# Kernel tuning notes

Hardware: AMD Instinct MI355X
Metric: run time of the kernel (lower is better)

## Reference

```python
import jax, jax.numpy as jnp
import numpy as np

DIM = 512
HEADS = 8
DIM_HEAD = 64
HIDDEN = HEADS * DIM_HEAD  # 512
SCALE = DIM_HEAD ** -0.5


def setup_inputs() -> dict:
    key = jax.random.key(0)
    k1, k2, k3 = jax.random.split(key, 3)
    x = jax.random.normal(k1, (4, 2048, DIM), dtype=jnp.float32)
    # torch Linear weight convention: [out_features, in_features], y = x @ W.T
    W_qkv = jax.random.normal(k2, (3 * HIDDEN, DIM), dtype=jnp.float32) * (DIM ** -0.5)
    W_out = jax.random.normal(k3, (DIM, HIDDEN), dtype=jnp.float32) * (HIDDEN ** -0.5)
    return {"x": x, "W_qkv": W_qkv, "W_out": W_out}


def reference(x, W_qkv, W_out):
    b, n, c = x.shape
    qkv = jnp.einsum('bnc,oc->bno', x, W_qkv)  # [b, n, 3*hidden]
    q, k, v = jnp.split(qkv, 3, axis=-1)
    # rearrange 'b n (h c) -> b h c n'
    def to_heads(t):
        return jnp.transpose(t.reshape(b, n, HEADS, DIM_HEAD), (0, 2, 3, 1))
    q, k, v = to_heads(q), to_heads(k), to_heads(v)
    q = q * SCALE
    sim = jnp.einsum('bhcn,bhcj->bhnj', q, k)  # [b, h, n, n]
    attn = jax.nn.softmax(sim, axis=-1)
    out = jnp.einsum('bhnj,bhdj->bhnd', attn, v)  # [b, h, n, d]
    out = jnp.transpose(out, (0, 2, 1, 3)).reshape(b, n, HIDDEN)  # 'b h n d -> b n (h d)'
    return jnp.einsum('bnh,oh->bno', out, W_out)
```

## Files before the change

kernel.cpp:

```cpp
#include <hip/hip_runtime.h>


typedef unsigned short u16;
typedef __attribute__((ext_vector_type(8))) short s16x8;
typedef __attribute__((ext_vector_type(4))) float f32x4;
typedef __attribute__((ext_vector_type(16))) float f32x16;

__device__ __forceinline__ u16 f2bf(float f) {
  unsigned int u = __float_as_uint(f);
  u = (u + 0x7fffu + ((u >> 16) & 1u)) >> 16;
  return (u16)u;
}

__device__ __forceinline__ void gload16(const u16* g, u16* lds_base) {
  __builtin_amdgcn_global_load_lds(
      (const __attribute__((address_space(1))) unsigned int*)g,
      (__attribute__((address_space(3))) unsigned int*)lds_base, 16, 0, 0);
}

__device__ __forceinline__ void permlane32_swap(unsigned& a, unsigned& b) {
  asm volatile("v_permlane32_swap_b32 %0, %1" : "+v"(a), "+v"(b));
}

__global__ __launch_bounds__(256) void cvt_all(
    const float* __restrict__ x, const float* __restrict__ w1,
    const float* __restrict__ w2, u16* __restrict__ xb,
    u16* __restrict__ w1b, u16* __restrict__ w2b) {
  constexpr int N1 = 8192 * 512 / 4, N2 = 1536 * 512 / 4, N3 = 512 * 512 / 4;
  int i = blockIdx.x * 256 + threadIdx.x;
  if (i >= N1 + N2 + N3) return;
  const float* src;
  u16* dst;
  int j;
  if (i < N1) { src = x; dst = xb; j = i; }
  else if (i < N1 + N2) { src = w1; dst = w1b; j = i - N1; }
  else { src = w2; dst = w2b; j = i - N1 - N2; }
  float4 f = ((const float4*)src)[j];
  uint2 o;
  o.x = (unsigned)f2bf(f.x) | ((unsigned)f2bf(f.y) << 16);
  o.y = (unsigned)f2bf(f.z) | ((unsigned)f2bf(f.w) << 16);
  ((uint2*)dst)[j] = o;
}

template <int BN, int MODE>
__global__ __launch_bounds__(256) void gemm128(
    const u16* __restrict__ A, const u16* __restrict__ B,
    float* __restrict__ Cf,
    u16* __restrict__ Qp, u16* __restrict__ Kp, u16* __restrict__ Vp) {
  constexpr int K = 512;
  constexpr int JN = BN / 32;
  __shared__ u16 smem[128 * 64 + BN * 64];
  u16* As = smem;
  u16* Bs = smem + 128 * 64;
  const int bm0 = blockIdx.x * 128, bn0 = blockIdx.y * BN;
  const int t = threadIdx.x, wave = t >> 6, lane = t & 63;
  const int quad = lane >> 4, l16 = lane & 15;
  const int wm = (wave & 1) * 64, wn = (wave >> 1) * (BN / 2);
  const int lr = lane >> 3, lc = lane & 7;
  const int swz = lc ^ lr;

  f32x4 acc[4][JN] = {};

  for (int k0 = 0; k0 < K; k0 += 64) {
    __syncthreads();
#pragma unroll
    for (int a = 0; a < 4; a++) {
      int r = wave * 32 + a * 8 + lr;
      gload16(A + (size_t)(bm0 + r) * K + k0 + swz * 8,
              &As[(wave * 32 + a * 8) * 64]);
    }
#pragma unroll
    for (int b = 0; b < BN / 32; b++) {
      int r = wave * (BN / 4) + b * 8 + lr;
      gload16(B + (size_t)(bn0 + r) * K + k0 + swz * 8,
              &Bs[(wave * (BN / 4) + b * 8) * 64]);
    }
    __syncthreads();
#pragma unroll
    for (int ks = 0; ks < 2; ks++) {
      s16x8 af[4], bf[JN];
#pragma unroll
      for (int i = 0; i < 4; i++) {
        int m = wm + i * 16 + l16;
        af[i] = *(const s16x8*)(&As[m * 64 + (((ks * 4 + quad) ^ (m & 7)) * 8)]);
      }
#pragma unroll
      for (int j = 0; j < JN; j++) {
        int n = wn + j * 16 + l16;
        bf[j] = *(const s16x8*)(&Bs[n * 64 + (((ks * 4 + quad) ^ (n & 7)) * 8)]);
      }
#pragma unroll
      for (int i = 0; i < 4; i++)
#pragma unroll
        for (int j = 0; j < JN; j++)
          acc[i][j] = __builtin_amdgcn_mfma_f32_16x16x32_bf16(af[i], bf[j], acc[i][j], 0, 0, 0);
    }
  }

  if constexpr (MODE == 1) {
#pragma unroll
    for (int i = 0; i < 4; i++)
#pragma unroll
      for (int j = 0; j < JN; j++)
#pragma unroll
        for (int r = 0; r < 4; r++) {
          int m = bm0 + wm + i * 16 + quad * 4 + r;
          int n = bn0 + wn + j * 16 + l16;
          Cf[(size_t)m * 512 + n] = acc[i][j][r];
        }
  } else {
    const int part = bn0 >> 9;
    if (part < 2) {
#pragma unroll
      for (int i = 0; i < 4; i++)
#pragma unroll
        for (int j = 0; j < JN; j++)
#pragma unroll
          for (int r = 0; r < 4; r++) {
            int m = bm0 + wm + i * 16 + quad * 4 + r;
            int n = bn0 + wn + j * 16 + l16;
            int oin = n & 511;
            int head = oin >> 6, dh = oin & 63;
            int bb = m >> 11, tok = m & 2047;
            size_t idx = ((size_t)(bb * 8 + head) * 2048 + tok) * 64 + dh;
            if (part == 0)
              Qp[idx] = f2bf(acc[i][j][r] * 0.18033688011112042f);
            else
              Kp[idx] = f2bf(acc[i][j][r]);
          }
    } else {
      __syncthreads();
#pragma unroll
      for (int i = 0; i < 4; i++)
#pragma unroll
        for (int j = 0; j < JN; j++)
#pragma unroll
          for (int r = 0; r < 4; r++) {
            int row = wm + i * 16 + quad * 4 + r;
            int cn = wn + j * 16 + l16;
            smem[row * 128 + (cn ^ (row & 7))] = f2bf(acc[i][j][r]);
          }
      __syncthreads();
      const int bb = bm0 >> 11;
      const int tokbase = bm0 & 2047;
      const int headbase = (bn0 & 511) >> 6;
#pragma unroll
      for (int it = 0; it < 8; it++) {
        int cn = it * 16 + (t >> 4);
        int dh = cn & 63, head = headbase + (cn >> 6);
        int tok0 = (t & 15) * 8;
        s16x8 pk;
#pragma unroll
        for (int k = 0; k < 8; k++) {
          int row = tok0 + k;
          pk[k] = (short)smem[row * 128 + (cn ^ (row & 7))];
        }
        *(s16x8*)(&Vp[((size_t)(bb * 8 + head) * 64 + dh) * 2048 + tokbase + tok0]) = pk;
      }
    }
  }
}

__global__ __launch_bounds__(256) void attn_kernel(
    const u16* __restrict__ Qg, const u16* __restrict__ Kg,
    const u16* __restrict__ Vtg, u16* __restrict__ Og) {
  __shared__ __attribute__((aligned(16))) u16 smem[3 * 64 * 72];
  u16* Qs = smem;
  u16* Ks = smem + 64 * 72;
  u16* Vt = smem + 2 * 64 * 72;
  float* Obuf = (float*)smem;
  float* Lbuf = (float*)((char*)smem + 64 * 68 * 4);

  const int bh = blockIdx.y;
  const int q0 = blockIdx.x * 64;
  const u16* Qh = Qg + (size_t)bh * 2048 * 64;
  const u16* Kh = Kg + (size_t)bh * 2048 * 64;
  const u16* Vh = Vtg + (size_t)bh * 64 * 2048;
  const int t = threadIdx.x, lane = t & 63, wave = t >> 6;
  const int wq = wave & 1, wk = wave >> 1;
  const int l32 = lane & 31, half = lane >> 5;
  const int srow = t >> 2, scolb = (t & 3) * 8;
  const int q = wq * 32 + l32;

#pragma unroll
  for (int p = 0; p < 2; p++) {
    int col = scolb + p * 32;
    *(s16x8*)(&Qs[srow * 72 + col]) = *(const s16x8*)(Qh + (size_t)(q0 + srow) * 64 + col);
  }
  __syncthreads();
  s16x8 bQ[4];
#pragma unroll
  for (int ks = 0; ks < 4; ks++)
    bQ[ks] = *(const s16x8*)(&Qs[q * 72 + ks * 16 + half * 8]);

  f32x16 o[2] = {};
  float l_acc = 0.f;

  for (int j0 = 0; j0 < 2048; j0 += 64) {
    __syncthreads();
#pragma unroll
    for (int p = 0; p < 2; p++) {
      int col = scolb + p * 32;
      *(s16x8*)(&Ks[srow * 72 + col]) = *(const s16x8*)(Kh + (size_t)(j0 + srow) * 64 + col);
      *(s16x8*)(&Vt[srow * 72 + col]) = *(const s16x8*)(Vh + (size_t)srow * 2048 + j0 + col);
    }
    __syncthreads();

    f32x16 s = {};
#pragma unroll
    for (int ks = 0; ks < 4; ks++) {
      s16x8 aK = *(const s16x8*)(&Ks[(wk * 32 + l32) * 72 + ks * 16 + half * 8]);
      s = __builtin_amdgcn_mfma_f32_32x32x16_bf16(aK, bQ[ks], s, 0, 0, 0);
    }

    unsigned pu[16];
#pragma unroll
    for (int r = 0; r < 16; r++) {
      float p = __builtin_amdgcn_exp2f(s[r]);
      unsigned u = __float_as_uint(p);
      l_acc += __uint_as_float(u & 0xffff0000u);
      pu[r] = u;
    }
    unsigned g[8];
#pragma unroll
    for (int v = 0; v < 8; v++)
      g[v] = __builtin_amdgcn_perm(pu[2 * v + 1], pu[2 * v], 0x07060302u);
    permlane32_swap(g[0], g[2]);
    permlane32_swap(g[1], g[3]);
    permlane32_swap(g[4], g[6]);
    permlane32_swap(g[5], g[7]);
    s16x8 bP[2];
    ((unsigned*)&bP[0])[0] = g[0]; ((unsigned*)&bP[0])[1] = g[1];
    ((unsigned*)&bP[0])[2] = g[2]; ((unsigned*)&bP[0])[3] = g[3];
    ((unsigned*)&bP[1])[0] = g[4]; ((unsigned*)&bP[1])[1] = g[5];
    ((unsigned*)&bP[1])[2] = g[6]; ((unsigned*)&bP[1])[3] = g[7];

#pragma unroll
    for (int dt = 0; dt < 2; dt++)
#pragma unroll
      for (int s2 = 0; s2 < 2; s2++) {
        s16x8 aV = *(const s16x8*)(&Vt[(dt * 32 + l32) * 72 + wk * 32 + s2 * 16 + half * 8]);
        o[dt] = __builtin_amdgcn_mfma_f32_32x32x16_bf16(aV, bP[s2], o[dt], 0, 0, 0);
      }
  }

  __syncthreads();
  Lbuf[(wk * 2 + half) * 64 + q] = l_acc;
  if (wk == 1) {
#pragma unroll
    for (int dt = 0; dt < 2; dt++)
#pragma unroll
      for (int gi = 0; gi < 4; gi++) {
        int d0 = 8 * gi + 4 * half + 32 * dt;
        float4 v = { o[dt][4 * gi + 0], o[dt][4 * gi + 1],
                     o[dt][4 * gi + 2], o[dt][4 * gi + 3] };
        *(float4*)(&Obuf[q * 68 + d0]) = v;
      }
  }
  __syncthreads();
  if (wk == 0) {
    float l = Lbuf[0 * 64 + q] + Lbuf[1 * 64 + q] + Lbuf[2 * 64 + q] + Lbuf[3 * 64 + q];
    float sc = __builtin_amdgcn_rcpf(l);
#pragma unroll
    for (int dt = 0; dt < 2; dt++)
#pragma unroll
      for (int gi = 0; gi < 4; gi++) {
        int d0 = 8 * gi + 4 * half + 32 * dt;
        float4 v = *(float4*)(&Obuf[q * 68 + d0]);
        v.x = (v.x + o[dt][4 * gi + 0]) * sc;
        v.y = (v.y + o[dt][4 * gi + 1]) * sc;
        v.z = (v.z + o[dt][4 * gi + 2]) * sc;
        v.w = (v.w + o[dt][4 * gi + 3]) * sc;
        *(float4*)(&Obuf[q * 68 + d0]) = v;
      }
  }
  __syncthreads();

  {
    const int bb = bh >> 3, h = bh & 7;
    int qq = t >> 2, d0 = (t & 3) * 16;
    float f[16];
#pragma unroll
    for (int c = 0; c < 4; c++) {
      float4 v = *(float4*)(&Obuf[qq * 68 + d0 + 4 * c]);
      f[4 * c + 0] = v.x; f[4 * c + 1] = v.y; f[4 * c + 2] = v.z; f[4 * c + 3] = v.w;
    }
    unsigned pk[8];
#pragma unroll
    for (int c = 0; c < 8; c++)
      pk[c] = (unsigned)f2bf(f[2 * c]) | ((unsigned)f2bf(f[2 * c + 1]) << 16);
    size_t base = ((size_t)bb * 2048 + q0 + qq) * 512 + h * 64 + d0;
    uint4 s0 = { pk[0], pk[1], pk[2], pk[3] };
    uint4 s1 = { pk[4], pk[5], pk[6], pk[7] };
    *(uint4*)(&Og[base]) = s0;
    *(uint4*)(&Og[base + 8]) = s1;
  }
}

extern "C" void kernel_launch(void* const* d_in, const int* in_sizes, int n_in,
                              void* d_out, int out_size, void* d_ws, size_t ws_size,
                              hipStream_t stream) {
  const float* x    = (const float*)d_in[0];
  const float* Wqkv = (const float*)d_in[1];
  const float* Wout = (const float*)d_in[2];
  float* y = (float*)d_out;

  char* ws = (char*)d_ws;
  size_t off = 0;
  auto alloc = [&](size_t bytes) {
    void* p = ws + off;
    off += (bytes + 255) & ~(size_t)255;
    return p;
  };
  u16* xb    = (u16*)alloc((size_t)8192 * 512 * 2);
  u16* wqkvb = (u16*)alloc((size_t)1536 * 512 * 2);
  u16* woutb = (u16*)alloc((size_t)512 * 512 * 2);
  u16* Qw    = (u16*)alloc((size_t)32 * 2048 * 64 * 2);
  u16* Kw    = (u16*)alloc((size_t)32 * 2048 * 64 * 2);
  u16* Vw    = (u16*)alloc((size_t)32 * 2048 * 64 * 2);
  u16* Ow    = (u16*)alloc((size_t)8192 * 512 * 2);
  if (off > ws_size) return;

  cvt_all<<<5120, 256, 0, stream>>>(x, Wqkv, Wout, xb, wqkvb, woutb);

  gemm128<128, 0><<<dim3(64, 12), 256, 0, stream>>>(xb, wqkvb, nullptr, Qw, Kw, Vw);
  attn_kernel<<<dim3(32, 32), 256, 0, stream>>>(Qw, Kw, Vw, Ow);
  gemm128<64, 1><<<dim3(64, 8), 256, 0, stream>>>(Ow, woutb, y, nullptr, nullptr, nullptr);
}
```

Before: 171.2 us.

## Restructure attention to 128-query blocks with direct global K/V loads and XCD mapping

The attention kernel now gives each wave its own 32 queries across the full key range, with 128 queries per block. K and V fragments are read straight from global memory instead of being staged through LDS behind two barriers per tile. The cross-wave output reduction is gone, and blocks are remapped so that heads sharing K/V land on the same XCD for L2 reuse. This removes per-tile synchronisation and LDS traffic, but depends on L1/L2 to serve repeated K/V reads across waves and halves the grid to 512 blocks.

```diff
diff --git a/kernel.cpp b/kernel.cpp
--- a/kernel.cpp
+++ b/kernel.cpp
@@ -164,136 +164,98 @@
 __global__ __launch_bounds__(256) void attn_kernel(
     const u16* __restrict__ Qg, const u16* __restrict__ Kg,
     const u16* __restrict__ Vtg, u16* __restrict__ Og) {
-  __shared__ __attribute__((aligned(16))) u16 smem[3 * 64 * 72];
-  u16* Qs = smem;
-  u16* Ks = smem + 64 * 72;
-  u16* Vt = smem + 2 * 64 * 72;
-  float* Obuf = (float*)smem;
-  float* Lbuf = (float*)((char*)smem + 64 * 68 * 4);
-
-  const int bh = blockIdx.y;
-  const int q0 = blockIdx.x * 64;
+  __shared__ __attribute__((aligned(16))) u16 Obuf[128 * 72];
+  __shared__ float Lw[2][128];
+  const int id = blockIdx.x;
+  const int xcd = id & 7, slot = id >> 3;
+  const int bh = xcd * 4 + (slot & 3);
+  const int q0 = (slot >> 2) * 128;
   const u16* Qh = Qg + (size_t)bh * 2048 * 64;
   const u16* Kh = Kg + (size_t)bh * 2048 * 64;
   const u16* Vh = Vtg + (size_t)bh * 64 * 2048;
-  const int t = threadIdx.x, lane = t & 63, wave = t >> 6;
-  const int wq = wave & 1, wk = wave >> 1;
+  const int t = threadIdx.x, lane = t & 63, w = t >> 6;
   const int l32 = lane & 31, half = lane >> 5;
-  const int srow = t >> 2, scolb = (t & 3) * 8;
-  const int q = wq * 32 + l32;
-
-#pragma unroll
-  for (int p = 0; p < 2; p++) {
-    int col = scolb + p * 32;
-    *(s16x8*)(&Qs[srow * 72 + col]) = *(const s16x8*)(Qh + (size_t)(q0 + srow) * 64 + col);
-  }
-  __syncthreads();
+  const int qrow = w * 32 + l32;
+
   s16x8 bQ[4];
 #pragma unroll
   for (int ks = 0; ks < 4; ks++)
-    bQ[ks] = *(const s16x8*)(&Qs[q * 72 + ks * 16 + half * 8]);
+    bQ[ks] = *(const s16x8*)(Qh + (size_t)(q0 + qrow) * 64 + ks * 16 + half * 8);
 
   f32x16 o[2] = {};
   float l_acc = 0.f;
 
+#pragma unroll 2
   for (int j0 = 0; j0 < 2048; j0 += 64) {
-    __syncthreads();
-#pragma unroll
-    for (int p = 0; p < 2; p++) {
-      int col = scolb + p * 32;
-      *(s16x8*)(&Ks[srow * 72 + col]) = *(const s16x8*)(Kh + (size_t)(j0 + srow) * 64 + col);
-      *(s16x8*)(&Vt[srow * 72 + col]) = *(const s16x8*)(Vh + (size_t)srow * 2048 + j0 + col);
-    }
-    __syncthreads();
-
-    f32x16 s = {};
-#pragma unroll
-    for (int ks = 0; ks < 4; ks++) {
-      s16x8 aK = *(const s16x8*)(&Ks[(wk * 32 + l32) * 72 + ks * 16 + half * 8]);
-      s = __builtin_amdgcn_mfma_f32_32x32x16_bf16(aK, bQ[ks], s, 0, 0, 0);
-    }
-
-    unsigned pu[16];
-#pragma unroll
-    for (int r = 0; r < 16; r++) {
-      float p = __builtin_amdgcn_exp2f(s[r]);
-      unsigned u = __float_as_uint(p);
-      l_acc += __uint_as_float(u & 0xffff0000u);
-      pu[r] = u;
-    }
-    unsigned g[8];
-#pragma unroll
-    for (int v = 0; v < 8; v++)
-      g[v] = __builtin_amdgcn_perm(pu[2 * v + 1], pu[2 * v], 0x07060302u);
-    permlane32_swap(g[0], g[2]);
-    permlane32_swap(g[1], g[3]);
-    permlane32_swap(g[4], g[6]);
-    permlane32_swap(g[5], g[7]);
-    s16x8 bP[2];
-    ((unsigned*)&bP[0])[0] = g[0]; ((unsigned*)&bP[0])[1] = g[1];
-    ((unsigned*)&bP[0])[2] = g[2]; ((unsigned*)&bP[0])[3] = g[3];
-    ((unsigned*)&bP[1])[0] = g[4]; ((unsigned*)&bP[1])[1] = g[5];
-    ((unsigned*)&bP[1])[2] = g[6]; ((unsigned*)&bP[1])[3] = g[7];
-
-#pragma unroll
-    for (int dt = 0; dt < 2; dt++)
-#pragma unroll
-      for (int s2 = 0; s2 < 2; s2++) {
-        s16x8 aV = *(const s16x8*)(&Vt[(dt * 32 + l32) * 72 + wk * 32 + s2 * 16 + half * 8]);
-        o[dt] = __builtin_amdgcn_mfma_f32_32x32x16_bf16(aV, bP[s2], o[dt], 0, 0, 0);
-      }
-  }
-
+#pragma unroll
+    for (int st = 0; st < 2; st++) {
+      const int jb = j0 + st * 32;
+      f32x16 s = {};
+#pragma unroll
+      for (int ks = 0; ks < 4; ks++) {
+        s16x8 aK = *(const s16x8*)(Kh + (size_t)(jb + l32) * 64 + ks * 16 + half * 8);
+        s = __builtin_amdgcn_mfma_f32_32x32x16_bf16(aK, bQ[ks], s, 0, 0, 0);
+      }
+      unsigned pu[16];
+#pragma unroll
+      for (int r = 0; r < 16; r++) {
+        float p = __builtin_amdgcn_exp2f(s[r]);
+        unsigned u = __float_as_uint(p);
+        l_acc += __uint_as_float(u & 0xffff0000u);
+        pu[r] = u;
+      }
+      unsigned g[8];
+#pragma unroll
+      for (int v = 0; v < 8; v++)
+        g[v] = __builtin_amdgcn_perm(pu[2 * v + 1], pu[2 * v], 0x07060302u);
+      permlane32_swap(g[0], g[2]);
+      permlane32_swap(g[1], g[3]);
+      permlane32_swap(g[4], g[6]);
+      permlane32_swap(g[5], g[7]);
+      s16x8 bP[2];
+      ((unsigned*)&bP[0])[0] = g[0]; ((unsigned*)&bP[0])[1] = g[1];
+      ((unsigned*)&bP[0])[2] = g[2]; ((unsigned*)&bP[0])[3] = g[3];
+      ((unsigned*)&bP[1])[0] = g[4]; ((unsigned*)&bP[1])[1] = g[5];
+      ((unsigned*)&bP[1])[2] = g[6]; ((unsigned*)&bP[1])[3] = g[7];
+
+#pragma unroll
+      for (int dt = 0; dt < 2; dt++)
+#pragma unroll
+        for (int s2 = 0; s2 < 2; s2++) {
+          s16x8 aV = *(const s16x8*)(Vh + (size_t)(dt * 32 + l32) * 2048
+                                     + jb + s2 * 16 + half * 8);
+          o[dt] = __builtin_amdgcn_mfma_f32_32x32x16_bf16(aV, bP[s2], o[dt], 0, 0, 0);
+        }
+    }
+  }
+
+  Lw[half][qrow] = l_acc;
   __syncthreads();
-  Lbuf[(wk * 2 + half) * 64 + q] = l_acc;
-  if (wk == 1) {
-#pragma unroll
-    for (int dt = 0; dt < 2; dt++)
-#pragma unroll
-      for (int gi = 0; gi < 4; gi++) {
-        int d0 = 8 * gi + 4 * half + 32 * dt;
-        float4 v = { o[dt][4 * gi + 0], o[dt][4 * gi + 1],
-                     o[dt][4 * gi + 2], o[dt][4 * gi + 3] };
-        *(float4*)(&Obuf[q * 68 + d0]) = v;
-      }
-  }
+  float l = l_acc + Lw[1 - half][qrow];
+  float sc = __builtin_amdgcn_rcpf(l);
+
+#pragma unroll
+  for (int dt = 0; dt < 2; dt++)
+#pragma unroll
+    for (int gi = 0; gi < 4; gi++) {
+      int d0 = 8 * gi + 4 * half + 32 * dt;
+      unsigned w0 = (unsigned)f2bf(o[dt][4 * gi + 0] * sc)
+                  | ((unsigned)f2bf(o[dt][4 * gi + 1] * sc) << 16);
+      unsigned w1 = (unsigned)f2bf(o[dt][4 * gi + 2] * sc)
+                  | ((unsigned)f2bf(o[dt][4 * gi + 3] * sc) << 16);
+      uint2 pk = { w0, w1 };
+      *(uint2*)(&Obuf[qrow * 72 + d0]) = pk;
+    }
   __syncthreads();
-  if (wk == 0) {
-    float l = Lbuf[0 * 64 + q] + Lbuf[1 * 64 + q] + Lbuf[2 * 64 + q] + Lbuf[3 * 64 + q];
-    float sc = __builtin_amdgcn_rcpf(l);
-#pragma unroll
-    for (int dt = 0; dt < 2; dt++)
-#pragma unroll
-      for (int gi = 0; gi < 4; gi++) {
-        int d0 = 8 * gi + 4 * half + 32 * dt;
-        float4 v = *(float4*)(&Obuf[q * 68 + d0]);
-        v.x = (v.x + o[dt][4 * gi + 0]) * sc;
-        v.y = (v.y + o[dt][4 * gi + 1]) * sc;
-        v.z = (v.z + o[dt][4 * gi + 2]) * sc;
-        v.w = (v.w + o[dt][4 * gi + 3]) * sc;
-        *(float4*)(&Obuf[q * 68 + d0]) = v;
-      }
-  }
-  __syncthreads();
-
   {
     const int bb = bh >> 3, h = bh & 7;
-    int qq = t >> 2, d0 = (t & 3) * 16;
-    float f[16];
+    int row = t >> 1, seg = (t & 1) * 32;
+    size_t base = ((size_t)bb * 2048 + q0 + row) * 512 + h * 64 + seg;
 #pragma unroll
     for (int c = 0; c < 4; c++) {
-      float4 v = *(float4*)(&Obuf[qq * 68 + d0 + 4 * c]);
-      f[4 * c + 0] = v.x; f[4 * c + 1] = v.y; f[4 * c + 2] = v.z; f[4 * c + 3] = v.w;
-    }
-    unsigned pk[8];
-#pragma unroll
-    for (int c = 0; c < 8; c++)
-      pk[c] = (unsigned)f2bf(f[2 * c]) | ((unsigned)f2bf(f[2 * c + 1]) << 16);
-    size_t base = ((size_t)bb * 2048 + q0 + qq) * 512 + h * 64 + d0;
-    uint4 s0 = { pk[0], pk[1], pk[2], pk[3] };
-    uint4 s1 = { pk[4], pk[5], pk[6], pk[7] };
-    *(uint4*)(&Og[base]) = s0;
-    *(uint4*)(&Og[base + 8]) = s1;
+      uint4 v = *(uint4*)(&Obuf[row * 72 + seg + c * 8]);
+      *(uint4*)(&Og[base + c * 8]) = v;
+    }
   }
 }
 
@@ -324,6 +286,6 @@
   cvt_all<<<5120, 256, 0, stream>>>(x, Wqkv, Wout, xb, wqkvb, woutb);
 
   gemm128<128, 0><<<dim3(64, 12), 256, 0, stream>>>(xb, wqkvb, nullptr, Qw, Kw, Vw);
-  attn_kernel<<<dim3(32, 32), 256, 0, stream>>>(Qw, Kw, Vw, Ow);
+  attn_kernel<<<512, 256, 0, stream>>>(Qw, Kw, Vw, Ow);
   gemm128<64, 1><<<dim3(64, 8), 256, 0, stream>>>(Ow, woutb, y, nullptr, nullptr, nullptr);
 }
```

Result: slower. 238.8 us (+39.5%).
